# Optimization experiments

Hardware: AMD Instinct MI355X
Metric: run time of the kernel (lower is better)

## Reference

```python
import jax, jax.numpy as jnp
import numpy as np

EPS = 1e-5
DN = ('NCHW', 'OIHW', 'NCHW')

def _conv(x, w):
    return jax.lax.conv_general_dilated(x, w, (1, 1), 'SAME', dimension_numbers=DN)

def _bn(x, g, b, m, v):
    scale = (g * jax.lax.rsqrt(v + EPS)).reshape(1, -1, 1, 1)
    shift = (b - m * g * jax.lax.rsqrt(v + EPS)).reshape(1, -1, 1, 1)
    return x * scale + shift

def _convbn(x, w, g, b, m, v):
    return jax.nn.relu(_bn(_conv(x, w), g, b, m, v))

def _top_pool(x):
    # CornerNet TopPool: out[..., i, :] = max over rows >= i (reverse cummax along H)
    return jax.lax.cummax(x, axis=2, reverse=True)

def _left_pool(x):
    # CornerNet LeftPool: out[..., :, j] = max over cols >= j (reverse cummax along W)
    return jax.lax.cummax(x, axis=3, reverse=True)

def _mk_convbn(key, cin, cout, k):
    ks = jax.random.split(key, 5)
    w = jax.random.normal(ks[0], (cout, cin, k, k), jnp.float32) * (1.0 / np.sqrt(cin * k * k))
    g = jax.random.uniform(ks[1], (cout,), jnp.float32, 0.5, 1.5)
    b = jax.random.normal(ks[2], (cout,), jnp.float32) * 0.1
    m = jax.random.normal(ks[3], (cout,), jnp.float32) * 0.1
    v = jax.random.uniform(ks[4], (cout,), jnp.float32, 0.5, 1.5)
    return w, g, b, m, v

def setup_inputs() -> dict:
    key = jax.random.key(0)
    ks = jax.random.split(key, 12)
    dim, mid, B, H, W = 256, 128, 8, 128, 128
    d = {}
    d['x'] = jax.random.normal(ks[0], (B, dim, H, W), jnp.float32)
    for name, kk in [('lc1', ks[1]), ('p1c1', ks[2]), ('lc2', ks[3]), ('p2c1', ks[4])]:
        w, g, b, m, v = _mk_convbn(kk, dim, mid, 3)
        d[name + '_w'], d[name + '_g'], d[name + '_b'], d[name + '_m'], d[name + '_v'] = w, g, b, m, v
    d['p1lc_w'] = jax.random.normal(ks[5], (mid, mid, 3, 3), jnp.float32) * (1.0 / np.sqrt(mid * 9))
    d['p2lc_w'] = jax.random.normal(ks[6], (mid, mid, 3, 3), jnp.float32) * (1.0 / np.sqrt(mid * 9))
    w, g, b, m, v = _mk_convbn(ks[7], mid, dim, 3)
    d['pconv1_w'], d['pbn1_g'], d['pbn1_b'], d['pbn1_m'], d['pbn1_v'] = w, g, b, m, v
    w, g, b, m, v = _mk_convbn(ks[8], dim, dim, 1)
    d['conv1_w'], d['bn1_g'], d['bn1_b'], d['bn1_m'], d['bn1_v'] = w, g, b, m, v
    w, g, b, m, v = _mk_convbn(ks[9], dim, dim, 3)
    d['c2_w'], d['c2_g'], d['c2_b'], d['c2_m'], d['c2_v'] = w, g, b, m, v
    return d

def reference(x, lc1_w, lc1_g, lc1_b, lc1_m, lc1_v, p1c1_w, p1c1_g, p1c1_b, p1c1_m, p1c1_v, lc2_w, lc2_g, lc2_b, lc2_m, lc2_v, p2c1_w, p2c1_g, p2c1_b, p2c1_m, p2c1_v, p1lc_w, p2lc_w, pconv1_w, pbn1_g, pbn1_b, pbn1_m, pbn1_v, conv1_w, bn1_g, bn1_b, bn1_m, bn1_v, c2_w, c2_g, c2_b, c2_m, c2_v):
    look_conv1 = _convbn(x, lc1_w, lc1_g, lc1_b, lc1_m, lc1_v)
    p1_conv1 = _convbn(x, p1c1_w, p1c1_g, p1c1_b, p1c1_m, p1c1_v)
    look2 = _left_pool(look_conv1)
    p1_look = _conv(p1_conv1 + look2, p1lc_w)
    pool1 = _top_pool(p1_look)
    look_conv2 = _convbn(x, lc2_w, lc2_g, lc2_b, lc2_m, lc2_v)
    p2_conv1 = _convbn(x, p2c1_w, p2c1_g, p2c1_b, p2c1_m, p2c1_v)
    look1 = _top_pool(look_conv2)
    p2_look = _conv(p2_conv1 + look1, p2lc_w)
    pool2 = _left_pool(p2_look)
    p_bn1 = _bn(_conv(pool1 + pool2, pconv1_w), pbn1_g, pbn1_b, pbn1_m, pbn1_v)
    bn1 = _bn(_conv(x, conv1_w), bn1_g, bn1_b, bn1_m, bn1_v)
    relu1 = jax.nn.relu(p_bn1 + bn1)
    return _convbn(relu1, c2_w, c2_g, c2_b, c2_m, c2_v)
```

## Files before the change

kernel.cpp:

```cpp
#include <hip/hip_runtime.h>
#include <hip/hip_bf16.h>
#include <stdint.h>
#include <math.h>

typedef __bf16 bf16;
typedef __bf16 bf16x8 __attribute__((ext_vector_type(8)));
typedef float f32x4 __attribute__((ext_vector_type(4)));


__global__ void k_x_split(const float* __restrict__ in, bf16* __restrict__ out) {
  __shared__ float t[32][33];
  const int b = blockIdx.z;
  const int p0 = blockIdx.x << 5, c0 = blockIdx.y << 5;
  const int tx = threadIdx.x, ty = threadIdx.y;
  const float* ib = in + (size_t)b * 256 * 16384;
  bf16* ob = out + (size_t)b * 16384 * 512;
#pragma unroll
  for (int k = 0; k < 32; k += 8)
    t[ty + k][tx] = ib[(size_t)(c0 + ty + k) * 16384 + p0 + tx];
  __syncthreads();
#pragma unroll
  for (int k = 0; k < 32; k += 8) {
    float v = t[tx][ty + k];
    bf16 hv = (bf16)v;
    bf16 lv = (bf16)(v - (float)hv);
    ob[(size_t)(p0 + ty + k) * 512 + c0 + tx] = hv;
    ob[(size_t)(p0 + ty + k) * 512 + 256 + c0 + tx] = lv;
  }
}

__global__ void k_repack2(const float* __restrict__ src, bf16* __restrict__ dst,
                          int Cout, int Cin, int taps, int coutTotal, int coff) {
  int tid = blockIdx.x * 256 + threadIdx.x;
  int total = Cout * Cin * taps;
  if (tid >= total) return;
  int t = tid % taps;
  int rest = tid / taps;
  int ci = rest % Cin;
  int co = rest / Cin;
  float w = src[tid];
  bf16 wh = (bf16)w;
  bf16 wl = (bf16)(w - (float)wh);
  int nchunk = Cin >> 5;
  size_t segsz = (size_t)coutTotal * Cin;
  size_t base = (((size_t)(2 * t) * nchunk + (ci >> 5)) * coutTotal + coff + co) * 32
                + (ci & 31);
  dst[base] = wh;
  dst[base + segsz] = wl;
}

__global__ void k_bncoef(const float* __restrict__ g, const float* __restrict__ b,
                         const float* __restrict__ m, const float* __restrict__ v,
                         float* __restrict__ sc, float* __restrict__ sh, int n) {
  int c = blockIdx.x * 256 + threadIdx.x;
  if (c >= n) return;
  float s = g[c] * (1.0f / sqrtf(v[c] + 1e-5f));
  sc[c] = s;
  sh[c] = b[c] - m[c] * s;
}

template <int NTAPS>
__global__ __launch_bounds__(256, 3)
void k_conv(const bf16* __restrict__ in, int Cin, int rowStride,
            const bf16* __restrict__ Wr, int Cout,
            const float* __restrict__ scale, const float* __restrict__ shift,
            const bf16* __restrict__ addbuf, int relu,
            int out_mode, void* __restrict__ out) {
  constexpr int R = (NTAPS == 9) ? 3 : 1;
  __shared__ bf16 b_slab[2 * R * 130 * 32];
  const int bx = blockIdx.x;
  const int bb = bx & 7, h = (bx >> 3) & 127;
  const int row = bb * 128 + h;
  const int co_block = blockIdx.y << 7;
  const int tid = threadIdx.x;
  const int lane = tid & 63, wave = tid >> 6;
  const int wm = (wave >> 1) << 6, wn = (wave & 1) << 6;
  const int quad = lane >> 4, l15 = lane & 15;
  const int nchunk = Cin >> 5;
  const size_t segsz = (size_t)Cout * Cin;

  f32x4 acc[4][4];
#pragma unroll
  for (int i = 0; i < 4; ++i)
#pragma unroll
    for (int j = 0; j < 4; ++j)
#pragma unroll
      for (int r = 0; r < 4; ++r) acc[i][j][r] = 0.0f;

  constexpr int nunits = 2 * R * 130;

  for (int cb = 0; cb < Cin; cb += 32) {
    for (int u = tid; u < nunits; u += 256) {
      int plane = u / 130, p = u - plane * 130;
      int hl, r;
      if (R == 3) { hl = plane >= 3; r = plane - (hl ? 3 : 0); }
      else        { hl = plane; r = 0; }
      int hi = h + r - (R == 3 ? 1 : 0);
      int wi = p - 1;
      uint4 v0, v1, v2, v3;
      v0.x = v0.y = v0.z = v0.w = 0u; v1 = v0; v2 = v0; v3 = v0;
      if ((unsigned)hi < 128u && (unsigned)wi < 128u) {
        const bf16* s = in + (size_t)((bb * 128 + hi) * 128 + wi) * rowStride
                        + (size_t)hl * Cin + cb;
        v0 = *(const uint4*)s;
        v1 = *(const uint4*)(s + 8);
        v2 = *(const uint4*)(s + 16);
        v3 = *(const uint4*)(s + 24);
      }
      bf16* d = &b_slab[(size_t)(plane * 130 + p) * 32];
      const int sw = (p >> 1) & 3;
      *(uint4*)(d + ((0 ^ sw) << 3)) = v0;
      *(uint4*)(d + ((1 ^ sw) << 3)) = v1;
      *(uint4*)(d + ((2 ^ sw) << 3)) = v2;
      *(uint4*)(d + ((3 ^ sw) << 3)) = v3;
    }
    __syncthreads();
#pragma unroll
    for (int tap = 0; tap < NTAPS; ++tap) {
      const int rr = (R == 3) ? (tap / 3) : 0;
      const int wc = (R == 3) ? (tap % 3) : 1;
      const int bH = rr * 130;
      const int bL = (R + rr) * 130;
      const int p0 = wn + l15 + wc;
      const int sw8 = (((p0 >> 1) & 3) ^ quad) << 3;
      const bf16* Ah = Wr + (((size_t)(2 * tap) * nchunk + (cb >> 5)) * Cout
                             + co_block + wm + l15) * 32 + quad * 8;
      const bf16* Al = Ah + segsz;
      bf16x8 afH[4], afL[4], bfH[4], bfL[4];
#pragma unroll
      for (int i = 0; i < 4; ++i) {
        afH[i] = *(const bf16x8*)(Ah + (size_t)i * 16 * 32);
        afL[i] = *(const bf16x8*)(Al + (size_t)i * 16 * 32);
      }
#pragma unroll
      for (int j = 0; j < 4; ++j) {
        const int p_idx = p0 + j * 16;
        bfH[j] = *(const bf16x8*)&b_slab[(size_t)(bH + p_idx) * 32 + sw8];
        bfL[j] = *(const bf16x8*)&b_slab[(size_t)(bL + p_idx) * 32 + sw8];
      }
#pragma unroll
      for (int i = 0; i < 4; ++i)
#pragma unroll
        for (int j = 0; j < 4; ++j) {
          acc[i][j] = __builtin_amdgcn_mfma_f32_16x16x32_bf16(afH[i], bfH[j], acc[i][j], 0, 0, 0);
          acc[i][j] = __builtin_amdgcn_mfma_f32_16x16x32_bf16(afH[i], bfL[j], acc[i][j], 0, 0, 0);
          acc[i][j] = __builtin_amdgcn_mfma_f32_16x16x32_bf16(afL[i], bfH[j], acc[i][j], 0, 0, 0);
        }
    }
    __syncthreads();
  }

#pragma unroll
  for (int i = 0; i < 4; ++i) {
    const int co = co_block + wm + i * 16 + (quad << 2);
#pragma unroll
    for (int j = 0; j < 4; ++j) {
      const int pos = wn + j * 16 + l15;
      float v[4];
#pragma unroll
      for (int r = 0; r < 4; ++r) v[r] = acc[i][j][r];
      if (scale) {
#pragma unroll
        for (int r = 0; r < 4; ++r) v[r] = v[r] * scale[co + r] + shift[co + r];
      }
      if (addbuf) {
        const bf16* ah = addbuf + (size_t)(row * 128 + pos) * (2 * Cout) + co;
        const bf16* al = ah + Cout;
#pragma unroll
        for (int r = 0; r < 4; ++r) v[r] += (float)ah[r] + (float)al[r];
      }
      if (relu) {
#pragma unroll
        for (int r = 0; r < 4; ++r) v[r] = fmaxf(v[r], 0.0f);
      }
      if (out_mode == 0) {
        bf16* ob = (bf16*)out;
        union { bf16 hv[4]; uint2 u; } ph, pl;
#pragma unroll
        for (int r = 0; r < 4; ++r) {
          ph.hv[r] = (bf16)v[r];
          pl.hv[r] = (bf16)(v[r] - (float)ph.hv[r]);
        }
        const size_t base = (size_t)(row * 128 + pos) * (2 * Cout);
        *(uint2*)&ob[base + co] = ph.u;
        *(uint2*)&ob[base + Cout + co] = pl.u;
      } else if (out_mode == 1) {
        float* of = (float*)out;
        float4 pk = make_float4(v[0], v[1], v[2], v[3]);
        *(float4*)&of[(size_t)(row * 128 + pos) * Cout + co] = pk;
      } else {
        float* of = (float*)out;
#pragma unroll
        for (int r = 0; r < 4; ++r)
          of[((size_t)(bb * Cout + co + r) * 128 + h) * 128 + pos] = v[r];
      }
    }
  }
}

__global__ void k_pool_s1(bf16* __restrict__ y) {
  int tid = blockIdx.x * 256 + threadIdx.x;
  int c = tid & 127, h = (tid >> 7) & 127, b = tid >> 14;
  bf16* base = y + (size_t)((b * 128 + h) * 128) * 512;
  float run = -INFINITY;
  for (int w = 127; w >= 0; --w) {
    bf16* p = base + (size_t)w * 512;
    float look = (float)p[c] + (float)p[256 + c];
    float padd = (float)p[128 + c] + (float)p[384 + c];
    run = fmaxf(run, look);
    float sum = run + padd;
    bf16 hv = (bf16)sum;
    p[c] = hv;
    p[128 + c] = (bf16)(sum - (float)hv);
  }
}
__global__ void k_pool_s2(bf16* __restrict__ y) {
  int tid = blockIdx.x * 256 + threadIdx.x;
  int c = tid & 127, w = (tid >> 7) & 127, b = tid >> 14;
  bf16* base = y + ((size_t)b * 16384 + w) * 512;
  float run = -INFINITY;
  for (int hh = 127; hh >= 0; --hh) {
    bf16* p = base + (size_t)hh * 65536;
    float look = (float)p[c] + (float)p[256 + c];
    float padd = (float)p[128 + c] + (float)p[384 + c];
    run = fmaxf(run, look);
    float sum = run + padd;
    bf16 hv = (bf16)sum;
    p[c] = hv;
    p[128 + c] = (bf16)(sum - (float)hv);
  }
}
__global__ void k_tpool_f(float* __restrict__ buf) {
  int tid = blockIdx.x * 256 + threadIdx.x;
  int c = tid & 127, w = (tid >> 7) & 127, b = tid >> 14;
  float* p = buf + ((size_t)b * 16384 + w) * 128 + c;
  float run = -INFINITY;
  for (int hh = 127; hh >= 0; --hh) {
    run = fmaxf(run, p[(size_t)hh * 16384]);
    p[(size_t)hh * 16384] = run;
  }
}
__global__ void k_lpool_add_f(const float* __restrict__ in, const float* __restrict__ addb,
                              bf16* __restrict__ out) {
  int tid = blockIdx.x * 256 + threadIdx.x;
  int c = tid & 127, h = (tid >> 7) & 127, b = tid >> 14;
  const float* p = in + (size_t)((b * 128 + h) * 128) * 128 + c;
  const float* a = addb + (size_t)((b * 128 + h) * 128) * 128 + c;
  bf16* o = out + (size_t)((b * 128 + h) * 128) * 256;
  float run = -INFINITY;
  for (int w = 127; w >= 0; --w) {
    run = fmaxf(run, p[(size_t)w * 128]);
    float sum = run + a[(size_t)w * 128];
    bf16 hv = (bf16)sum;
    o[(size_t)w * 256 + c] = hv;
    o[(size_t)w * 256 + 128 + c] = (bf16)(sum - (float)hv);
  }
}

extern "C" void kernel_launch(void* const* d_in, const int* in_sizes, int n_in,
                              void* d_out, int out_size, void* d_ws, size_t ws_size,
                              hipStream_t stream) {
  (void)in_sizes; (void)n_in; (void)out_size; (void)ws_size;
#define INF(i) ((const float*)d_in[i])
  char* ws = (char*)d_ws;
  const size_t MB = 1 << 20;
  bf16* wrA  = (bf16*)(ws + 0);
  bf16* wrB  = (bf16*)(ws + 2359296);
  bf16* wrp1 = (bf16*)(ws + 4718592);
  bf16* wrp2 = (bf16*)(ws + 5308416);
  bf16* wrpc = (bf16*)(ws + 5898240);
  bf16* wrc1 = (bf16*)(ws + 7077888);
  bf16* wrc2 = (bf16*)(ws + 7340032);
  float* scA  = (float*)(ws + 9699328);
  float* shA  = (float*)(ws + 9703424);
  float* scB  = (float*)(ws + 9707520);
  float* shB  = (float*)(ws + 9711616);
  float* scp  = (float*)(ws + 9715712);
  float* shp  = (float*)(ws + 9719808);
  float* scb  = (float*)(ws + 9723904);
  float* shb  = (float*)(ws + 9728000);
  float* scc2 = (float*)(ws + 9732096);
  float* shc2 = (float*)(ws + 9736192);
  bf16*  x_hl  = (bf16*)(ws + 10 * MB);
  bf16*  bnrel = (bf16*)(ws + 138 * MB);
  float* p1lk  = (float*)(ws + 266 * MB);
  float* p2lk  = (float*)(ws + 10 * MB);
  bf16*  psum  = (bf16*)(ws + 74 * MB);
  bf16*  yscr  = (bf16*)d_out;

  k_x_split<<<dim3(512, 8, 8), dim3(32, 8), 0, stream>>>(INF(0), x_hl);

  k_repack2<<<1152, 256, 0, stream>>>(INF(1),  wrA,  128, 256, 9, 256, 0);
  k_repack2<<<1152, 256, 0, stream>>>(INF(6),  wrA,  128, 256, 9, 256, 128);
  k_repack2<<<1152, 256, 0, stream>>>(INF(11), wrB,  128, 256, 9, 256, 0);
  k_repack2<<<1152, 256, 0, stream>>>(INF(16), wrB,  128, 256, 9, 256, 128);
  k_repack2<<<576,  256, 0, stream>>>(INF(21), wrp1, 128, 128, 9, 128, 0);
  k_repack2<<<576,  256, 0, stream>>>(INF(22), wrp2, 128, 128, 9, 128, 0);
  k_repack2<<<1152, 256, 0, stream>>>(INF(23), wrpc, 256, 128, 9, 256, 0);
  k_repack2<<<256,  256, 0, stream>>>(INF(28), wrc1, 256, 256, 1, 256, 0);
  k_repack2<<<2304, 256, 0, stream>>>(INF(33), wrc2, 256, 256, 9, 256, 0);

  k_bncoef<<<1, 256, 0, stream>>>(INF(2),  INF(3),  INF(4),  INF(5),  scA,       shA,       128);
  k_bncoef<<<1, 256, 0, stream>>>(INF(7),  INF(8),  INF(9),  INF(10), scA + 128, shA + 128, 128);
  k_bncoef<<<1, 256, 0, stream>>>(INF(12), INF(13), INF(14), INF(15), scB,       shB,       128);
  k_bncoef<<<1, 256, 0, stream>>>(INF(17), INF(18), INF(19), INF(20), scB + 128, shB + 128, 128);
  k_bncoef<<<1, 256, 0, stream>>>(INF(24), INF(25), INF(26), INF(27), scp, shp, 256);
  k_bncoef<<<1, 256, 0, stream>>>(INF(29), INF(30), INF(31), INF(32), scb, shb, 256);
  k_bncoef<<<1, 256, 0, stream>>>(INF(34), INF(35), INF(36), INF(37), scc2, shc2, 256);

  k_conv<1><<<dim3(1024, 2), 256, 0, stream>>>(x_hl, 256, 512, wrc1, 256, scb, shb, nullptr, 0, 0, bnrel);
  k_conv<9><<<dim3(1024, 2), 256, 0, stream>>>(x_hl, 256, 512, wrA, 256, scA, shA, nullptr, 1, 0, yscr);
  k_pool_s1<<<512, 256, 0, stream>>>(yscr);
  k_conv<9><<<dim3(1024, 1), 256, 0, stream>>>(yscr, 128, 512, wrp1, 128, nullptr, nullptr, nullptr, 0, 1, p1lk);
  k_conv<9><<<dim3(1024, 2), 256, 0, stream>>>(x_hl, 256, 512, wrB, 256, scB, shB, nullptr, 1, 0, yscr);
  k_pool_s2<<<512, 256, 0, stream>>>(yscr);
  k_conv<9><<<dim3(1024, 1), 256, 0, stream>>>(yscr, 128, 512, wrp2, 128, nullptr, nullptr, nullptr, 0, 1, p2lk);
  k_tpool_f<<<512, 256, 0, stream>>>(p1lk);
  k_lpool_add_f<<<512, 256, 0, stream>>>(p2lk, p1lk, psum);
  k_conv<9><<<dim3(1024, 2), 256, 0, stream>>>(psum, 128, 256, wrpc, 256, scp, shp, bnrel, 1, 0, bnrel);
  k_conv<9><<<dim3(1024, 2), 256, 0, stream>>>(bnrel, 256, 512, wrc2, 256, scc2, shc2, nullptr, 1, 2, (float*)d_out);
#undef INF
}
```

Baseline: 2.401 ms.

## Switch conv GEMM from 16x16x32 to 32x32x16 MFMA tiles

The conv kernel's per-wave 64x64 tile now uses 2x2 tiles of the 32x32x16 bf16 MFMA instead of 4x4 tiles of 16x16x32. The weight repack layout is split into 16-channel K halves to match the new A-operand fragment shape, and the LDS B-operand reads and epilogue indexing are remapped. The larger MFMA does more work per instruction and needs fewer fragment loads per multiply, which is meant to raise matrix-core throughput. In exchange it changes register and accumulator layout and the LDS bank access pattern.

```diff
diff --git a/kernel.cpp b/kernel.cpp
--- a/kernel.cpp
+++ b/kernel.cpp
@@ -5,7 +5,7 @@
 
 typedef __bf16 bf16;
 typedef __bf16 bf16x8 __attribute__((ext_vector_type(8)));
-typedef float f32x4 __attribute__((ext_vector_type(4)));
+typedef float f32x16 __attribute__((ext_vector_type(16)));
 
 
 __global__ void k_x_split(const float* __restrict__ in, bf16* __restrict__ out) {
@@ -43,8 +43,8 @@
   bf16 wl = (bf16)(w - (float)wh);
   int nchunk = Cin >> 5;
   size_t segsz = (size_t)coutTotal * Cin;
-  size_t base = (((size_t)(2 * t) * nchunk + (ci >> 5)) * coutTotal + coff + co) * 32
-                + (ci & 31);
+  size_t base = ((((size_t)(2 * t) * nchunk + (ci >> 5)) * 2 + ((ci >> 4) & 1)) * coutTotal
+                 + coff + co) * 16 + (ci & 15);
   dst[base] = wh;
   dst[base + segsz] = wl;
 }
@@ -75,17 +75,17 @@
   const int tid = threadIdx.x;
   const int lane = tid & 63, wave = tid >> 6;
   const int wm = (wave >> 1) << 6, wn = (wave & 1) << 6;
-  const int quad = lane >> 4, l15 = lane & 15;
+  const int col = lane & 31, kg = lane >> 5;
   const int nchunk = Cin >> 5;
   const size_t segsz = (size_t)Cout * Cin;
 
-  f32x4 acc[4][4];
-#pragma unroll
-  for (int i = 0; i < 4; ++i)
-#pragma unroll
-    for (int j = 0; j < 4; ++j)
-#pragma unroll
-      for (int r = 0; r < 4; ++r) acc[i][j][r] = 0.0f;
+  f32x16 acc[2][2];
+#pragma unroll
+  for (int i = 0; i < 2; ++i)
+#pragma unroll
+    for (int j = 0; j < 2; ++j)
+#pragma unroll
+      for (int r = 0; r < 16; ++r) acc[i][j][r] = 0.0f;
 
   constexpr int nunits = 2 * R * 130;
 
@@ -121,81 +121,87 @@
       const int wc = (R == 3) ? (tap % 3) : 1;
       const int bH = rr * 130;
       const int bL = (R + rr) * 130;
-      const int p0 = wn + l15 + wc;
-      const int sw8 = (((p0 >> 1) & 3) ^ quad) << 3;
-      const bf16* Ah = Wr + (((size_t)(2 * tap) * nchunk + (cb >> 5)) * Cout
-                             + co_block + wm + l15) * 32 + quad * 8;
-      const bf16* Al = Ah + segsz;
-      bf16x8 afH[4], afL[4], bfH[4], bfL[4];
-#pragma unroll
-      for (int i = 0; i < 4; ++i) {
-        afH[i] = *(const bf16x8*)(Ah + (size_t)i * 16 * 32);
-        afL[i] = *(const bf16x8*)(Al + (size_t)i * 16 * 32);
-      }
-#pragma unroll
-      for (int j = 0; j < 4; ++j) {
-        const int p_idx = p0 + j * 16;
-        bfH[j] = *(const bf16x8*)&b_slab[(size_t)(bH + p_idx) * 32 + sw8];
-        bfL[j] = *(const bf16x8*)&b_slab[(size_t)(bL + p_idx) * 32 + sw8];
-      }
-#pragma unroll
-      for (int i = 0; i < 4; ++i)
-#pragma unroll
-        for (int j = 0; j < 4; ++j) {
-          acc[i][j] = __builtin_amdgcn_mfma_f32_16x16x32_bf16(afH[i], bfH[j], acc[i][j], 0, 0, 0);
-          acc[i][j] = __builtin_amdgcn_mfma_f32_16x16x32_bf16(afH[i], bfL[j], acc[i][j], 0, 0, 0);
-          acc[i][j] = __builtin_amdgcn_mfma_f32_16x16x32_bf16(afL[i], bfH[j], acc[i][j], 0, 0, 0);
-        }
+      const bf16* A0 = Wr + ((((size_t)(2 * tap) * nchunk + (cb >> 5)) * 2) * Cout
+                             + co_block + wm + col) * 16 + kg * 8;
+      bf16x8 afH[2][2], afL[2][2], bfH[2][2], bfL[2][2];
+#pragma unroll
+      for (int ti = 0; ti < 2; ++ti)
+#pragma unroll
+        for (int kh = 0; kh < 2; ++kh) {
+          const bf16* a = A0 + (size_t)kh * Cout * 16 + ti * 32 * 16;
+          afH[ti][kh] = *(const bf16x8*)a;
+          afL[ti][kh] = *(const bf16x8*)(a + segsz);
+        }
+#pragma unroll
+      for (int tj = 0; tj < 2; ++tj)
+#pragma unroll
+        for (int kh = 0; kh < 2; ++kh) {
+          const int p = wn + tj * 32 + col + wc;
+          const int slot = ((kh << 1) + kg) ^ ((p >> 1) & 3);
+          bfH[tj][kh] = *(const bf16x8*)&b_slab[(size_t)(bH + p) * 32 + slot * 8];
+          bfL[tj][kh] = *(const bf16x8*)&b_slab[(size_t)(bL + p) * 32 + slot * 8];
+        }
+#pragma unroll
+      for (int ti = 0; ti < 2; ++ti)
+#pragma unroll
+        for (int tj = 0; tj < 2; ++tj)
+#pragma unroll
+          for (int kh = 0; kh < 2; ++kh) {
+            acc[ti][tj] = __builtin_amdgcn_mfma_f32_32x32x16_bf16(afH[ti][kh], bfH[tj][kh], acc[ti][tj], 0, 0, 0);
+            acc[ti][tj] = __builtin_amdgcn_mfma_f32_32x32x16_bf16(afH[ti][kh], bfL[tj][kh], acc[ti][tj], 0, 0, 0);
+            acc[ti][tj] = __builtin_amdgcn_mfma_f32_32x32x16_bf16(afL[ti][kh], bfH[tj][kh], acc[ti][tj], 0, 0, 0);
+          }
     }
     __syncthreads();
   }
 
 #pragma unroll
-  for (int i = 0; i < 4; ++i) {
-    const int co = co_block + wm + i * 16 + (quad << 2);
-#pragma unroll
-    for (int j = 0; j < 4; ++j) {
-      const int pos = wn + j * 16 + l15;
-      float v[4];
-#pragma unroll
-      for (int r = 0; r < 4; ++r) v[r] = acc[i][j][r];
-      if (scale) {
-#pragma unroll
-        for (int r = 0; r < 4; ++r) v[r] = v[r] * scale[co + r] + shift[co + r];
+  for (int ti = 0; ti < 2; ++ti)
+#pragma unroll
+    for (int tj = 0; tj < 2; ++tj)
+#pragma unroll
+      for (int g = 0; g < 4; ++g) {
+        const int co = co_block + wm + ti * 32 + g * 8 + kg * 4;
+        const int pos = wn + tj * 32 + col;
+        float v[4];
+#pragma unroll
+        for (int r = 0; r < 4; ++r) v[r] = acc[ti][tj][g * 4 + r];
+        if (scale) {
+#pragma unroll
+          for (int r = 0; r < 4; ++r) v[r] = v[r] * scale[co + r] + shift[co + r];
+        }
+        if (addbuf) {
+          const bf16* ah = addbuf + (size_t)(row * 128 + pos) * (2 * Cout) + co;
+          const bf16* al = ah + Cout;
+#pragma unroll
+          for (int r = 0; r < 4; ++r) v[r] += (float)ah[r] + (float)al[r];
+        }
+        if (relu) {
+#pragma unroll
+          for (int r = 0; r < 4; ++r) v[r] = fmaxf(v[r], 0.0f);
+        }
+        if (out_mode == 0) {
+          bf16* ob = (bf16*)out;
+          union { bf16 hv[4]; uint2 u; } ph, pl;
+#pragma unroll
+          for (int r = 0; r < 4; ++r) {
+            ph.hv[r] = (bf16)v[r];
+            pl.hv[r] = (bf16)(v[r] - (float)ph.hv[r]);
+          }
+          const size_t base = (size_t)(row * 128 + pos) * (2 * Cout);
+          *(uint2*)&ob[base + co] = ph.u;
+          *(uint2*)&ob[base + Cout + co] = pl.u;
+        } else if (out_mode == 1) {
+          float* of = (float*)out;
+          float4 pk = make_float4(v[0], v[1], v[2], v[3]);
+          *(float4*)&of[(size_t)(row * 128 + pos) * Cout + co] = pk;
+        } else {
+          float* of = (float*)out;
+#pragma unroll
+          for (int r = 0; r < 4; ++r)
+            of[((size_t)(bb * Cout + co + r) * 128 + h) * 128 + pos] = v[r];
+        }
       }
-      if (addbuf) {
-        const bf16* ah = addbuf + (size_t)(row * 128 + pos) * (2 * Cout) + co;
-        const bf16* al = ah + Cout;
-#pragma unroll
-        for (int r = 0; r < 4; ++r) v[r] += (float)ah[r] + (float)al[r];
-      }
-      if (relu) {
-#pragma unroll
-        for (int r = 0; r < 4; ++r) v[r] = fmaxf(v[r], 0.0f);
-      }
-      if (out_mode == 0) {
-        bf16* ob = (bf16*)out;
-        union { bf16 hv[4]; uint2 u; } ph, pl;
-#pragma unroll
-        for (int r = 0; r < 4; ++r) {
-          ph.hv[r] = (bf16)v[r];
-          pl.hv[r] = (bf16)(v[r] - (float)ph.hv[r]);
-        }
-        const size_t base = (size_t)(row * 128 + pos) * (2 * Cout);
-        *(uint2*)&ob[base + co] = ph.u;
-        *(uint2*)&ob[base + Cout + co] = pl.u;
-      } else if (out_mode == 1) {
-        float* of = (float*)out;
-        float4 pk = make_float4(v[0], v[1], v[2], v[3]);
-        *(float4*)&of[(size_t)(row * 128 + pos) * Cout + co] = pk;
-      } else {
-        float* of = (float*)out;
-#pragma unroll
-        for (int r = 0; r < 4; ++r)
-          of[((size_t)(bb * Cout + co + r) * 128 + h) * 128 + pos] = v[r];
-      }
-    }
-  }
 }
 
 __global__ void k_pool_s1(bf16* __restrict__ y) {
```

Result: slower. 2.826 ms (+17.7%).
